# Kernel tuning notes

Measured on AMD Instinct MI355X. Metric: run time of the kernel, lower is better.

The kernel has to match this reference:

```python
import jax, jax.numpy as jnp
import numpy as np

SM_SCALE = 0.08838834764831845  # 1/sqrt(128)
Q_LEN, K_LEN, H, M, D = 1024, 1024, 8, 8, 128


def setup_inputs() -> dict:
    key = jax.random.key(0)
    k1, k2, k3, k4 = jax.random.split(key, 4)
    Q = jax.random.normal(k1, (Q_LEN, H, M, D), dtype=jnp.float32)
    K_expanded = jax.random.normal(k2, (K_LEN, H, M, D), dtype=jnp.float32)
    mask = jax.random.normal(k3, (Q_LEN, K_LEN), dtype=jnp.float32)
    sinks = jax.random.normal(k4, (H, M, Q_LEN, 1), dtype=jnp.float32)
    return {"Q": Q, "K_expanded": K_expanded, "mask": mask, "sinks": sinks}


def reference(Q, K_expanded, mask, sinks):
    # [h, m, q, k] scaled scores + additive mask
    QK = jnp.einsum('qhmd,khmd->hmqk', Q, K_expanded) * SM_SCALE
    QK = QK + mask[None, None, :, :]
    # append sink logits on the key axis -> [h, m, q, k+1]
    return jnp.concatenate([QK, sinks], axis=-1)
```

## Files before the change

### kernel.cpp

```cpp
#include <hip/hip_runtime.h>
#include <hip/hip_bf16.h>

#define QL 1024
#define KL 1024
#define HM 64
#define DD 128
#define SM_SCALE 0.08838834764831845f

#define BM 128
#define BN 128
#define LDPAD 136

typedef __bf16 bf16x8 __attribute__((ext_vector_type(8)));
typedef __bf16 bf16x4 __attribute__((ext_vector_type(4)));
typedef float floatx4 __attribute__((ext_vector_type(4)));

__global__ __launch_bounds__(256, 2)
void qk_kernel(const float* __restrict__ Qg, const float* __restrict__ Kg,
               const float* __restrict__ mask, float* __restrict__ out)
{
    const int g    = blockIdx.y;
    const int tile = blockIdx.x;
    const int qt = (tile >> 3) * BM;
    const int kt = (tile & 7) * BN;

    __shared__ __bf16 As[BM][LDPAD];
    __shared__ __bf16 Bs[BN][LDPAD];

    const int t = threadIdx.x;

    const float* Ag = Qg + (size_t)qt * (HM * DD) + (size_t)g * DD;
    const float* Bg = Kg + (size_t)kt * (HM * DD) + (size_t)g * DD;
#pragma unroll
    for (int j = 0; j < 16; ++j) {
        int c = t + 256 * j;
        int row = c >> 5;
        int c4  = c & 31;
        float4 a = *(const float4*)(Ag + (size_t)row * (HM * DD) + c4 * 4);
        float4 b = *(const float4*)(Bg + (size_t)row * (HM * DD) + c4 * 4);
        bf16x4 av = { (__bf16)a.x, (__bf16)a.y, (__bf16)a.z, (__bf16)a.w };
        bf16x4 bv = { (__bf16)b.x, (__bf16)b.y, (__bf16)b.z, (__bf16)b.w };
        *(bf16x4*)&As[row][c4 * 4] = av;
        *(bf16x4*)&Bs[row][c4 * 4] = bv;
    }
    __syncthreads();

    const int wave = t >> 6;
    const int lane = t & 63;
    const int wm = (wave & 1) * 64;
    const int wn = (wave >> 1) * 64;
    const int lr = lane & 15;
    const int quad = lane >> 4;

    floatx4 acc[4][4] = {};

#pragma unroll
    for (int ks = 0; ks < 4; ++ks) {
        const int d0 = ks * 32 + quad * 8;
        bf16x8 af[4], bf[4];
#pragma unroll
        for (int mi = 0; mi < 4; ++mi)
            af[mi] = *(const bf16x8*)&As[wm + mi * 16 + lr][d0];
#pragma unroll
        for (int ni = 0; ni < 4; ++ni)
            bf[ni] = *(const bf16x8*)&Bs[wn + ni * 16 + lr][d0];
#pragma unroll
        for (int mi = 0; mi < 4; ++mi)
#pragma unroll
            for (int ni = 0; ni < 4; ++ni)
                acc[mi][ni] = __builtin_amdgcn_mfma_f32_16x16x32_bf16(
                    af[mi], bf[ni], acc[mi][ni], 0, 0, 0);
    }

    const size_t obase = (size_t)g * QL * 1025;
#pragma unroll
    for (int mi = 0; mi < 4; ++mi) {
#pragma unroll
        for (int r = 0; r < 4; ++r) {
            int q = qt + wm + mi * 16 + quad * 4 + r;
            const float* mrow = mask + (size_t)q * KL;
            float* orow = out + obase + (size_t)q * 1025;
#pragma unroll
            for (int ni = 0; ni < 4; ++ni) {
                int k = kt + wn + ni * 16 + lr;
                orow[k] = acc[mi][ni][r] * SM_SCALE + mrow[k];
            }
        }
    }
}

__global__ void sink_kernel(const float* __restrict__ sinks, float* __restrict__ out)
{
    int idx = blockIdx.x * 256 + threadIdx.x;
    out[(size_t)idx * 1025 + 1024] = sinks[idx];
}

extern "C" void kernel_launch(void* const* d_in, const int* in_sizes, int n_in,
                              void* d_out, int out_size, void* d_ws, size_t ws_size,
                              hipStream_t stream)
{
    const float* Q     = (const float*)d_in[0];
    const float* K     = (const float*)d_in[1];
    const float* mask  = (const float*)d_in[2];
    const float* sinks = (const float*)d_in[3];
    float* out = (float*)d_out;

    sink_kernel<<<(HM * QL) / 256, 256, 0, stream>>>(sinks, out);
    qk_kernel<<<dim3(64, 64), 256, 0, stream>>>(Q, K, mask, out);
}
```

Baseline: 412.5 us.

## Pre-convert Q/K to bf16 tiled layout and load tiles via global_load_lds

Adds a prep kernel that converts Q and K to bf16 once and stores them in a chunked tile layout in workspace. The main kernel then fills LDS with direct global-to-LDS loads instead of re-reading fp32 for every tile, swaps the MFMA operands so each lane writes four contiguous output floats with vectorized mask reads, fuses the sink write into the last k-tile, and reorders block IDs for locality. This removes the repeated fp32 Q/K reads (each tile was read 8 times), but adds an extra kernel launch and a workspace round trip. It falls back to the old path when the workspace is too small.

```diff
diff --git a/kernel.cpp b/kernel.cpp
--- a/kernel.cpp
+++ b/kernel.cpp
@@ -1,5 +1,6 @@
 #include <hip/hip_runtime.h>
 #include <hip/hip_bf16.h>
+#include <stdint.h>
 
 #define QL 1024
 #define KL 1024
@@ -7,13 +8,120 @@
 #define DD 128
 #define SM_SCALE 0.08838834764831845f
 
+typedef __bf16 bf16x8 __attribute__((ext_vector_type(8)));
+typedef __bf16 bf16x4 __attribute__((ext_vector_type(4)));
+typedef float floatx4 __attribute__((ext_vector_type(4)));
+
+typedef __attribute__((address_space(1))) const uint32_t gl_u32;
+typedef __attribute__((address_space(3))) uint32_t lds_u32;
+
+__global__ __launch_bounds__(256)
+void prep_kernel(const float* __restrict__ Q, const float* __restrict__ K,
+                 __bf16* __restrict__ ws)
+{
+    const int tid = blockIdx.x * 256 + threadIdx.x;
+    const float* src = (tid >> 20) ? K : Q;
+    __bf16* dst = ws + ((size_t)(tid >> 20) << 23);
+    const int rem = tid & 0xFFFFF;
+    const int c  = rem & 15;
+    const int r  = (rem >> 4) & 127;
+    const int rt = (rem >> 11) & 7;
+    const int g  = rem >> 14;
+    const int row = rt * 128 + r;
+
+    const float* s = src + (((size_t)row * HM + g) << 7) + (c << 3);
+    float4 a = *(const float4*)s;
+    float4 b = *(const float4*)(s + 4);
+    bf16x8 v = { (__bf16)a.x, (__bf16)a.y, (__bf16)a.z, (__bf16)a.w,
+                 (__bf16)b.x, (__bf16)b.y, (__bf16)b.z, (__bf16)b.w };
+    const size_t dchunk = ((size_t)(g * 8 + rt) * 16 + c) * 128 + r;
+    *(bf16x8*)(dst + dchunk * 8) = v;
+}
+
+__global__ __launch_bounds__(256, 2)
+void qk2_kernel(const __bf16* __restrict__ ws, const float* __restrict__ mask,
+                const float* __restrict__ sinks, float* __restrict__ out)
+{
+    const int bid  = blockIdx.x;
+    const int lin  = bid >> 3;
+    const int g    = ((bid & 7) << 3) + (lin >> 6);
+    const int tile = lin & 63;
+    const int qt = tile >> 3;
+    const int kt = tile & 7;
+
+    __shared__ __bf16 As[16384];
+    __shared__ __bf16 Bs[16384];
+
+    const int t    = threadIdx.x;
+    const int wave = t >> 6;
+    const int lane = t & 63;
+
+    const __bf16* Aso = ws + ((size_t)(g * 8 + qt) << 14);
+    const __bf16* Bso = ws + ((size_t)1 << 23) + ((size_t)(g * 8 + kt) << 14);
+
+    {
+        const char* ga = (const char*)Aso + wave * 1024 + lane * 16;
+        const char* gb = (const char*)Bso + wave * 1024 + lane * 16;
+        char* la = (char*)As + wave * 1024;
+        char* lb = (char*)Bs + wave * 1024;
+#pragma unroll
+        for (int j = 0; j < 8; ++j) {
+            __builtin_amdgcn_global_load_lds((gl_u32*)(ga + j * 4096),
+                                             (lds_u32*)(la + j * 4096), 16, 0, 0);
+            __builtin_amdgcn_global_load_lds((gl_u32*)(gb + j * 4096),
+                                             (lds_u32*)(lb + j * 4096), 16, 0, 0);
+        }
+    }
+    __syncthreads();
+
+    const int wm   = (wave & 1) << 6;
+    const int wn   = (wave >> 1) << 6;
+    const int lr   = lane & 15;
+    const int quad = lane >> 4;
+
+    floatx4 acc[4][4] = {};
+#pragma unroll
+    for (int ks = 0; ks < 4; ++ks) {
+        const int cb = ((ks << 2) + quad) << 7;
+        bf16x8 af[4], bfr[4];
+#pragma unroll
+        for (int mi = 0; mi < 4; ++mi)
+            af[mi] = *(const bf16x8*)&As[(size_t)(cb + wm + mi * 16 + lr) << 3];
+#pragma unroll
+        for (int ni = 0; ni < 4; ++ni)
+            bfr[ni] = *(const bf16x8*)&Bs[(size_t)(cb + wn + ni * 16 + lr) << 3];
+#pragma unroll
+        for (int mi = 0; mi < 4; ++mi)
+#pragma unroll
+            for (int ni = 0; ni < 4; ++ni)
+                acc[mi][ni] = __builtin_amdgcn_mfma_f32_16x16x32_bf16(
+                    bfr[ni], af[mi], acc[mi][ni], 0, 0, 0);
+    }
+
+    const size_t obase = (size_t)g * QL * 1025;
+#pragma unroll
+    for (int mi = 0; mi < 4; ++mi) {
+        const int q = (qt << 7) + wm + mi * 16 + lr;
+        const float* mrow = mask + ((size_t)q << 10);
+        float* orow = out + obase + (size_t)q * 1025;
+#pragma unroll
+        for (int ni = 0; ni < 4; ++ni) {
+            const int k0 = (kt << 7) + wn + ni * 16 + (quad << 2);
+            floatx4 mv = *(const floatx4*)(mrow + k0);
+            floatx4 v  = acc[mi][ni] * SM_SCALE + mv;
+            __builtin_memcpy((void*)(orow + k0), &v, 16);
+        }
+    }
+
+    if (kt == 7 && t < 128) {
+        const int q = (qt << 7) + t;
+        out[obase + (size_t)q * 1025 + 1024] = sinks[(g << 10) + q];
+    }
+}
+
 #define BM 128
 #define BN 128
 #define LDPAD 136
-
-typedef __bf16 bf16x8 __attribute__((ext_vector_type(8)));
-typedef __bf16 bf16x4 __attribute__((ext_vector_type(4)));
-typedef float floatx4 __attribute__((ext_vector_type(4)));
 
 __global__ __launch_bounds__(256, 2)
 void qk_kernel(const float* __restrict__ Qg, const float* __restrict__ Kg,
@@ -24,11 +132,10 @@
     const int qt = (tile >> 3) * BM;
     const int kt = (tile & 7) * BN;
 
-    __shared__ __bf16 As[BM][LDPAD];
-    __shared__ __bf16 Bs[BN][LDPAD];
+    __shared__ __bf16 Asf[BM][LDPAD];
+    __shared__ __bf16 Bsf[BN][LDPAD];
 
     const int t = threadIdx.x;
-
     const float* Ag = Qg + (size_t)qt * (HM * DD) + (size_t)g * DD;
     const float* Bg = Kg + (size_t)kt * (HM * DD) + (size_t)g * DD;
 #pragma unroll
@@ -40,8 +147,8 @@
         float4 b = *(const float4*)(Bg + (size_t)row * (HM * DD) + c4 * 4);
         bf16x4 av = { (__bf16)a.x, (__bf16)a.y, (__bf16)a.z, (__bf16)a.w };
         bf16x4 bv = { (__bf16)b.x, (__bf16)b.y, (__bf16)b.z, (__bf16)b.w };
-        *(bf16x4*)&As[row][c4 * 4] = av;
-        *(bf16x4*)&Bs[row][c4 * 4] = bv;
+        *(bf16x4*)&Asf[row][c4 * 4] = av;
+        *(bf16x4*)&Bsf[row][c4 * 4] = bv;
     }
     __syncthreads();
 
@@ -53,17 +160,16 @@
     const int quad = lane >> 4;
 
     floatx4 acc[4][4] = {};
-
 #pragma unroll
     for (int ks = 0; ks < 4; ++ks) {
         const int d0 = ks * 32 + quad * 8;
         bf16x8 af[4], bf[4];
 #pragma unroll
         for (int mi = 0; mi < 4; ++mi)
-            af[mi] = *(const bf16x8*)&As[wm + mi * 16 + lr][d0];
+            af[mi] = *(const bf16x8*)&Asf[wm + mi * 16 + lr][d0];
 #pragma unroll
         for (int ni = 0; ni < 4; ++ni)
-            bf[ni] = *(const bf16x8*)&Bs[wn + ni * 16 + lr][d0];
+            bf[ni] = *(const bf16x8*)&Bsf[wn + ni * 16 + lr][d0];
 #pragma unroll
         for (int mi = 0; mi < 4; ++mi)
 #pragma unroll
@@ -105,6 +211,12 @@
     const float* sinks = (const float*)d_in[3];
     float* out = (float*)d_out;
 
-    sink_kernel<<<(HM * QL) / 256, 256, 0, stream>>>(sinks, out);
-    qk_kernel<<<dim3(64, 64), 256, 0, stream>>>(Q, K, mask, out);
-}
+    if (d_ws && ws_size >= (size_t)(2u * 8388608u * sizeof(__bf16))) {
+        __bf16* ws = (__bf16*)d_ws;
+        prep_kernel<<<8192, 256, 0, stream>>>(Q, K, ws);
+        qk2_kernel<<<4096, 256, 0, stream>>>(ws, mask, sinks, out);
+    } else {
+        sink_kernel<<<(HM * QL) / 256, 256, 0, stream>>>(sinks, out);
+        qk_kernel<<<dim3(64, 64), 256, 0, stream>>>(Q, K, mask, out);
+    }
+}
```

Measured after the change: 395.7 us. -4.1%, faster.

## Keep Q tile resident, stream double-buffered K tiles, fuse sink write

Applied to the files above, without the earlier changes.

Each block now loads one 128-row Q tile once and loops over sixteen 64-row K tiles, using double-buffered shared memory with register prefetch of the next K tile. Swapping the MFMA operands lets each lane write four contiguous floats, so mask loads and output stores are vectorised. Block indices are remapped so each group of heads stays on one XCD, and the separate sink kernel is folded into the main kernel. The grid shrinks from 4096 to 512 blocks, which lowers parallelism and latency hiding in exchange for less redundant Q loading and conversion.

```diff
diff --git a/kernel.cpp b/kernel.cpp
--- a/kernel.cpp
+++ b/kernel.cpp
@@ -1,98 +1,125 @@
 #include <hip/hip_runtime.h>
 #include <hip/hip_bf16.h>
+#include <stdint.h>
 
 #define QL 1024
 #define KL 1024
 #define HM 64
 #define DD 128
 #define SM_SCALE 0.08838834764831845f
-
-#define BM 128
-#define BN 128
-#define LDPAD 136
+#define LDP 136
 
 typedef __bf16 bf16x8 __attribute__((ext_vector_type(8)));
 typedef __bf16 bf16x4 __attribute__((ext_vector_type(4)));
 typedef float floatx4 __attribute__((ext_vector_type(4)));
 
 __global__ __launch_bounds__(256, 2)
-void qk_kernel(const float* __restrict__ Qg, const float* __restrict__ Kg,
-               const float* __restrict__ mask, float* __restrict__ out)
+void qk3_kernel(const float* __restrict__ Qg, const float* __restrict__ Kg,
+                const float* __restrict__ mask, const float* __restrict__ sinks,
+                float* __restrict__ out)
 {
-    const int g    = blockIdx.y;
-    const int tile = blockIdx.x;
-    const int qt = (tile >> 3) * BM;
-    const int kt = (tile & 7) * BN;
+    const int bid   = blockIdx.x;
+    const int xcd   = bid & 7;
+    const int inner = bid >> 3;
+    const int qt    = inner & 7;
+    const int g     = xcd * 8 + (inner >> 3);
 
-    __shared__ __bf16 As[BM][LDPAD];
-    __shared__ __bf16 Bs[BN][LDPAD];
+    __shared__ __bf16 Qs[128][LDP];
+    __shared__ __bf16 Ks[2][64][LDP];
 
     const int t = threadIdx.x;
 
-    const float* Ag = Qg + (size_t)qt * (HM * DD) + (size_t)g * DD;
-    const float* Bg = Kg + (size_t)kt * (HM * DD) + (size_t)g * DD;
+    const float* Qbase = Qg + (size_t)(qt * 128) * (HM * DD) + (size_t)g * DD;
+    const float* Kbase = Kg + (size_t)g * DD;
 #pragma unroll
     for (int j = 0; j < 16; ++j) {
         int c = t + 256 * j;
-        int row = c >> 5;
-        int c4  = c & 31;
-        float4 a = *(const float4*)(Ag + (size_t)row * (HM * DD) + c4 * 4);
-        float4 b = *(const float4*)(Bg + (size_t)row * (HM * DD) + c4 * 4);
+        int row = c >> 5, c4 = c & 31;
+        float4 a = *(const float4*)(Qbase + (size_t)row * (HM * DD) + c4 * 4);
         bf16x4 av = { (__bf16)a.x, (__bf16)a.y, (__bf16)a.z, (__bf16)a.w };
+        *(bf16x4*)&Qs[row][c4 * 4] = av;
+    }
+#pragma unroll
+    for (int j = 0; j < 8; ++j) {
+        int c = t + 256 * j;
+        int row = c >> 5, c4 = c & 31;
+        float4 b = *(const float4*)(Kbase + (size_t)row * (HM * DD) + c4 * 4);
         bf16x4 bv = { (__bf16)b.x, (__bf16)b.y, (__bf16)b.z, (__bf16)b.w };
-        *(bf16x4*)&As[row][c4 * 4] = av;
-        *(bf16x4*)&Bs[row][c4 * 4] = bv;
+        *(bf16x4*)&Ks[0][row][c4 * 4] = bv;
     }
     __syncthreads();
 
     const int wave = t >> 6;
     const int lane = t & 63;
-    const int wm = (wave & 1) * 64;
-    const int wn = (wave >> 1) * 64;
-    const int lr = lane & 15;
+    const int wm   = (wave & 1) * 64;
+    const int wnk  = (wave >> 1) * 32;
+    const int lr   = lane & 15;
     const int quad = lane >> 4;
 
-    floatx4 acc[4][4] = {};
+    const size_t obase = (size_t)g * QL * 1025;
+
+    for (int kt = 0; kt < 16; ++kt) {
+        const int b = kt & 1;
+
+        float4 nf[8];
+        if (kt < 15) {
+            const float* nb = Kg + (size_t)((kt + 1) * 64) * (HM * DD) + (size_t)g * DD;
+#pragma unroll
+            for (int j = 0; j < 8; ++j) {
+                int c = t + 256 * j;
+                nf[j] = *(const float4*)(nb + (size_t)(c >> 5) * (HM * DD) + (c & 31) * 4);
+            }
+        }
+
+        floatx4 acc[4][2] = {};
+#pragma unroll
+        for (int ks = 0; ks < 4; ++ks) {
+            const int d0 = ks * 32 + quad * 8;
+            bf16x8 af[4], bfr[2];
+#pragma unroll
+            for (int mi = 0; mi < 4; ++mi)
+                af[mi] = *(const bf16x8*)&Qs[wm + mi * 16 + lr][d0];
+#pragma unroll
+            for (int ni = 0; ni < 2; ++ni)
+                bfr[ni] = *(const bf16x8*)&Ks[b][wnk + ni * 16 + lr][d0];
+#pragma unroll
+            for (int mi = 0; mi < 4; ++mi)
+#pragma unroll
+                for (int ni = 0; ni < 2; ++ni)
+                    acc[mi][ni] = __builtin_amdgcn_mfma_f32_16x16x32_bf16(
+                        bfr[ni], af[mi], acc[mi][ni], 0, 0, 0);
+        }
 
 #pragma unroll
-    for (int ks = 0; ks < 4; ++ks) {
-        const int d0 = ks * 32 + quad * 8;
-        bf16x8 af[4], bf[4];
+        for (int mi = 0; mi < 4; ++mi) {
+            const int q = (qt << 7) + wm + mi * 16 + lr;
+            const float* mrow = mask + ((size_t)q << 10);
+            float* orow = out + obase + (size_t)q * 1025;
 #pragma unroll
-        for (int mi = 0; mi < 4; ++mi)
-            af[mi] = *(const bf16x8*)&As[wm + mi * 16 + lr][d0];
+            for (int ni = 0; ni < 2; ++ni) {
+                const int k0 = (kt << 6) + wnk + ni * 16 + (quad << 2);
+                floatx4 mv = *(const floatx4*)(mrow + k0);
+                floatx4 v  = acc[mi][ni] * SM_SCALE + mv;
+                __builtin_memcpy((void*)(orow + k0), &v, 16);
+            }
+        }
+
+        if (kt < 15) {
 #pragma unroll
-        for (int ni = 0; ni < 4; ++ni)
-            bf[ni] = *(const bf16x8*)&Bs[wn + ni * 16 + lr][d0];
-#pragma unroll
-        for (int mi = 0; mi < 4; ++mi)
-#pragma unroll
-            for (int ni = 0; ni < 4; ++ni)
-                acc[mi][ni] = __builtin_amdgcn_mfma_f32_16x16x32_bf16(
-                    af[mi], bf[ni], acc[mi][ni], 0, 0, 0);
+            for (int j = 0; j < 8; ++j) {
+                int c = t + 256 * j;
+                bf16x4 bv = { (__bf16)nf[j].x, (__bf16)nf[j].y,
+                              (__bf16)nf[j].z, (__bf16)nf[j].w };
+                *(bf16x4*)&Ks[1 - b][c >> 5][(c & 31) * 4] = bv;
+            }
+            __syncthreads();
+        }
     }
 
-    const size_t obase = (size_t)g * QL * 1025;
-#pragma unroll
-    for (int mi = 0; mi < 4; ++mi) {
-#pragma unroll
-        for (int r = 0; r < 4; ++r) {
-            int q = qt + wm + mi * 16 + quad * 4 + r;
-            const float* mrow = mask + (size_t)q * KL;
-            float* orow = out + obase + (size_t)q * 1025;
-#pragma unroll
-            for (int ni = 0; ni < 4; ++ni) {
-                int k = kt + wn + ni * 16 + lr;
-                orow[k] = acc[mi][ni][r] * SM_SCALE + mrow[k];
-            }
-        }
+    if (t < 128) {
+        const int q = (qt << 7) + t;
+        out[obase + (size_t)q * 1025 + 1024] = sinks[((size_t)g << 10) + q];
     }
-}
-
-__global__ void sink_kernel(const float* __restrict__ sinks, float* __restrict__ out)
-{
-    int idx = blockIdx.x * 256 + threadIdx.x;
-    out[(size_t)idx * 1025 + 1024] = sinks[idx];
 }
 
 extern "C" void kernel_launch(void* const* d_in, const int* in_sizes, int n_in,
@@ -105,6 +132,5 @@
     const float* sinks = (const float*)d_in[3];
     float* out = (float*)d_out;
 
-    sink_kernel<<<(HM * QL) / 256, 256, 0, stream>>>(sinks, out);
-    qk_kernel<<<dim3(64, 64), 256, 0, stream>>>(Q, K, mask, out);
+    qk3_kernel<<<512, 256, 0, stream>>>(Q, K, mask, sinks, out);
 }
```

Result: no change. 418.7 us (+1.5%).
